# Optimization experiments

Hardware: AMD Instinct MI355X
Metric: run time of the kernel (lower is better)

The kernel has to match this reference:

```python
import jax, jax.numpy as jnp
import numpy as np

MODEL_DIM = 1024
NUM_HEADS = 16
HEAD_DIM = MODEL_DIM // NUM_HEADS


def setup_inputs() -> dict:
    key = jax.random.key(0)
    ks = jax.random.split(key, 9)
    s = 1.0 / np.sqrt(MODEL_DIM)
    d = {
        "query": jax.random.normal(ks[0], (2, 2048, MODEL_DIM), dtype=jnp.float32),
        "Wq": jax.random.normal(ks[1], (MODEL_DIM, MODEL_DIM), dtype=jnp.float32) * s,
        "bq": jnp.zeros((MODEL_DIM,), dtype=jnp.float32),
        "Wk": jax.random.normal(ks[2], (MODEL_DIM, MODEL_DIM), dtype=jnp.float32) * s,
        "bk": jnp.zeros((MODEL_DIM,), dtype=jnp.float32),
        "Wv": jax.random.normal(ks[3], (MODEL_DIM, MODEL_DIM), dtype=jnp.float32) * s,
        "bv": jnp.zeros((MODEL_DIM,), dtype=jnp.float32),
        "Wo": jax.random.normal(ks[4], (MODEL_DIM, MODEL_DIM), dtype=jnp.float32) * s,
        "bo": jnp.zeros((MODEL_DIM,), dtype=jnp.float32),
    }
    return d


def reference(query, Wq, bq, Wk, bk, Wv, bv, Wo, bo):
    B, S, D = query.shape
    H, hd = NUM_HEADS, HEAD_DIM
    # self-attention: key = value = query
    q = (query @ Wq.T + bq).reshape(B, S, H, hd).transpose(0, 2, 1, 3)  # [B,H,S,hd]
    k = (query @ Wk.T + bk).reshape(B, S, H, hd).transpose(0, 2, 1, 3)
    v = (query @ Wv.T + bv).reshape(B, S, H, hd).transpose(0, 2, 1, 3)
    scores = jnp.einsum("bhqd,bhkd->bhqk", q, k) / np.sqrt(hd)  # [B,H,S,S]
    attn = jax.nn.softmax(scores, axis=-1)
    ctx = jnp.einsum("bhqk,bhkd->bhqd", attn, v)  # [B,H,S,hd]
    ctx = ctx.transpose(0, 2, 1, 3).reshape(B, S, D)
    return ctx @ Wo.T + bo
```

## Files before the change

### kernel.cpp

```cpp
#include <hip/hip_runtime.h>

typedef __attribute__((ext_vector_type(8))) __bf16 bf16x8;
typedef __attribute__((ext_vector_type(8))) unsigned short ushort8;
typedef __attribute__((ext_vector_type(4))) unsigned short ushort4v;
typedef __attribute__((ext_vector_type(4))) float f32x4;
typedef __attribute__((ext_vector_type(2))) _Float16 f16x2;
typedef __attribute__((ext_vector_type(4))) _Float16 f16x4;
typedef __attribute__((ext_vector_type(8))) _Float16 f16x8;
typedef __attribute__((ext_vector_type(2))) __fp16 fp16v2;

__device__ __forceinline__ unsigned short f2bf(float f) {
    union { float f; unsigned int u; } c; c.f = f;
    unsigned int u = c.u;
    u += 0x7fffu + ((u >> 16) & 1u);
    return (unsigned short)(u >> 16);
}

__device__ __forceinline__ void async16(const void* g, void* l) {
    __builtin_amdgcn_global_load_lds(
        (const __attribute__((address_space(1))) unsigned int*)g,
        (__attribute__((address_space(3))) unsigned int*)l, 16, 0, 0);
}

__global__ __launch_bounds__(256) void cvt_all(
    const float* __restrict__ q,  const float* __restrict__ wq,
    const float* __restrict__ wk, const float* __restrict__ wv,
    const float* __restrict__ wo,
    unsigned short* __restrict__ q_bf, unsigned short* __restrict__ wqkv,
    unsigned short* __restrict__ wo_bf, float scale_k)
{
    const int NQ = 4096 * 1024, NW = 1024 * 1024;
    int i = (blockIdx.x * 256 + threadIdx.x) * 4;
    const float* src; unsigned short* dst; float sc = 1.0f; int off;
    if (i < NQ)               { src = q;  dst = q_bf;          off = i; }
    else if (i < NQ + NW)     { src = wq; dst = wqkv;          off = i - NQ; }
    else if (i < NQ + 2 * NW) { src = wk; dst = wqkv + NW;     off = i - NQ - NW; sc = scale_k; }
    else if (i < NQ + 3 * NW) { src = wv; dst = wqkv + 2 * NW; off = i - NQ - 2 * NW; }
    else                      { src = wo; dst = wo_bf;         off = i - NQ - 3 * NW; }
    float4 v = *(const float4*)(src + off);
    ushort4v o;
    o[0] = f2bf(v.x * sc); o[1] = f2bf(v.y * sc);
    o[2] = f2bf(v.z * sc); o[3] = f2bf(v.w * sc);
    *(ushort4v*)(dst + off) = o;
}

__global__ __launch_bounds__(256) void qkv_gemm(
    const unsigned short* __restrict__ A,
    const unsigned short* __restrict__ B,
    unsigned short* __restrict__ qkv,
    _Float16* __restrict__ vtg,
    const float* __restrict__ b0, const float* __restrict__ b1, const float* __restrict__ b2,
    float s1)
{
    __shared__ __align__(16) unsigned short As[128 * 64];
    __shared__ __align__(16) unsigned short Bs[128 * 64];

    const int tid  = threadIdx.x;
    const int lane = tid & 63, wave = tid >> 6;
    const int quad = lane >> 4, l15 = lane & 15;
    const int wm = wave >> 1, wn = wave & 1;
    const int by = blockIdx.y, bx = blockIdx.x;
    const int K = 1024;

    const int srow = lane >> 3;
    const int sp   = lane & 7;
    const int scl  = sp ^ srow;
    const int sw   = l15 & 7;

    f32x4 acc[4][4];
#pragma unroll
    for (int i = 0; i < 4; ++i)
#pragma unroll
        for (int j = 0; j < 4; ++j) acc[i][j] = (f32x4)(0.0f);

    for (int kt = 0; kt < 16; ++kt) {
        __syncthreads();
#pragma unroll
        for (int j = 0; j < 4; ++j) {
            int r0 = wave * 32 + j * 8;
            async16(A + (size_t)(by * 128 + r0 + srow) * K + kt * 64 + scl * 8, &As[r0 * 64]);
            async16(B + (size_t)(bx * 128 + r0 + srow) * K + kt * 64 + scl * 8, &Bs[r0 * 64]);
        }
        __syncthreads();

#pragma unroll
        for (int kh = 0; kh < 2; ++kh) {
            bf16x8 af[4], bfr[4];
#pragma unroll
            for (int mi = 0; mi < 4; ++mi)
                af[mi] = __builtin_bit_cast(bf16x8,
                    *(const ushort8*)&As[(wm * 64 + mi * 16 + l15) * 64 + ((kh * 4 + quad) ^ sw) * 8]);
#pragma unroll
            for (int ni = 0; ni < 4; ++ni)
                bfr[ni] = __builtin_bit_cast(bf16x8,
                    *(const ushort8*)&Bs[(wn * 64 + ni * 16 + l15) * 64 + ((kh * 4 + quad) ^ sw) * 8]);
#pragma unroll
            for (int mi = 0; mi < 4; ++mi)
#pragma unroll
                for (int ni = 0; ni < 4; ++ni)
                    acc[mi][ni] = __builtin_amdgcn_mfma_f32_16x16x32_bf16(af[mi], bfr[ni], acc[mi][ni], 0, 0, 0);
        }
    }

    if (bx < 16) {
#pragma unroll
        for (int ni = 0; ni < 4; ++ni) {
            int n = bx * 128 + wn * 64 + ni * 16 + l15;
            float bias = (n < 1024) ? b0[n] : b1[n - 1024] * s1;
#pragma unroll
            for (int mi = 0; mi < 4; ++mi) {
#pragma unroll
                for (int r = 0; r < 4; ++r) {
                    int m = by * 128 + wm * 64 + mi * 16 + quad * 4 + r;
                    qkv[(size_t)m * 2048 + n] = f2bf(acc[mi][ni][r] + bias);
                }
            }
        }
    } else {
        const int mb = by * 128 + wm * 64;
        const int b  = mb >> 11;
        const int st = (mb & 2047) >> 6;
#pragma unroll
        for (int ni = 0; ni < 4; ++ni) {
            int vf = (bx - 16) * 128 + wn * 64 + ni * 16 + l15;
            int h = vf >> 6, hd = vf & 63;
            float bias = b2[vf];
            _Float16* vrow = vtg + ((size_t)((b * 16 + h) * 64 + hd)) * 2048 + st * 64;
#pragma unroll
            for (int mi = 0; mi < 4; ++mi) {
                int p = ((mi >> 1) * 4 + quad) ^ (l15 & 7);
                f16x4 o;
#pragma unroll
                for (int r = 0; r < 4; ++r) o[r] = (_Float16)(acc[mi][ni][r] + bias);
                *(f16x4*)(vrow + p * 8 + (mi & 1) * 4) = o;
            }
        }
    }
}

__global__ __launch_bounds__(256) void out_gemm(
    const unsigned short* __restrict__ A,
    const unsigned short* __restrict__ B,
    float* __restrict__ Cout,
    const float* __restrict__ bo)
{
    __shared__ __align__(16) unsigned short As[128 * 64];
    __shared__ __align__(16) unsigned short Bs[64 * 64];

    const int tid  = threadIdx.x;
    const int lane = tid & 63, wave = tid >> 6;
    const int quad = lane >> 4, l15 = lane & 15;
    const int wm = wave >> 1, wn = wave & 1;
    const int by = blockIdx.y, bx = blockIdx.x;
    const int K = 1024;

    const int srow = lane >> 3;
    const int sp   = lane & 7;
    const int scl  = sp ^ srow;
    const int sw   = l15 & 7;

    f32x4 acc[4][2];
#pragma unroll
    for (int i = 0; i < 4; ++i)
#pragma unroll
        for (int j = 0; j < 2; ++j) acc[i][j] = (f32x4)(0.0f);

    for (int kt = 0; kt < 16; ++kt) {
        __syncthreads();
#pragma unroll
        for (int j = 0; j < 4; ++j) {
            int r0 = wave * 32 + j * 8;
            async16(A + (size_t)(by * 128 + r0 + srow) * K + kt * 64 + scl * 8, &As[r0 * 64]);
        }
#pragma unroll
        for (int j = 0; j < 2; ++j) {
            int r0 = wave * 16 + j * 8;
            async16(B + (size_t)(bx * 64 + r0 + srow) * K + kt * 64 + scl * 8, &Bs[r0 * 64]);
        }
        __syncthreads();

#pragma unroll
        for (int kh = 0; kh < 2; ++kh) {
            bf16x8 af[4], bfr[2];
#pragma unroll
            for (int mi = 0; mi < 4; ++mi)
                af[mi] = __builtin_bit_cast(bf16x8,
                    *(const ushort8*)&As[(wm * 64 + mi * 16 + l15) * 64 + ((kh * 4 + quad) ^ sw) * 8]);
#pragma unroll
            for (int ni = 0; ni < 2; ++ni)
                bfr[ni] = __builtin_bit_cast(bf16x8,
                    *(const ushort8*)&Bs[(wn * 32 + ni * 16 + l15) * 64 + ((kh * 4 + quad) ^ sw) * 8]);
#pragma unroll
            for (int mi = 0; mi < 4; ++mi)
#pragma unroll
                for (int ni = 0; ni < 2; ++ni)
                    acc[mi][ni] = __builtin_amdgcn_mfma_f32_16x16x32_bf16(af[mi], bfr[ni], acc[mi][ni], 0, 0, 0);
        }
    }

#pragma unroll
    for (int ni = 0; ni < 2; ++ni) {
        int n = bx * 64 + wn * 32 + ni * 16 + l15;
        float bias = bo[n];
#pragma unroll
        for (int mi = 0; mi < 4; ++mi) {
#pragma unroll
            for (int r = 0; r < 4; ++r) {
                int m = by * 128 + wm * 64 + mi * 16 + quad * 4 + r;
                Cout[(size_t)m * 1024 + n] = acc[mi][ni][r] + bias;
            }
        }
    }
}

__global__ __launch_bounds__(256, 2) void attn(const unsigned short* __restrict__ qkv,
                                               const _Float16* __restrict__ vtg,
                                               unsigned short* __restrict__ ctx)
{
    __shared__ __align__(16) char smem[65536];

    const int tid  = threadIdx.x;
    const int lane = tid & 63, wave = tid >> 6;
    const int quad = lane >> 4, l15 = lane & 15;
    const int bh = blockIdx.y;
    const int b = bh >> 4, h = bh & 15;
    const int q0 = blockIdx.x * 64;

    const int srow = lane >> 3;
    const int sp   = lane & 7;
    const int scl  = sp ^ srow;
    const int sw   = l15 & 7;

    unsigned short* KsW = (unsigned short*)(smem + wave * 16384);
    _Float16*       VtW = (_Float16*)(smem + wave * 16384 + 8192);

    bf16x8 qf[4][2];
#pragma unroll
    for (int s = 0; s < 4; ++s) {
        int qrow = b * 2048 + q0 + s * 16 + l15;
#pragma unroll
        for (int kh = 0; kh < 2; ++kh)
            qf[s][kh] = __builtin_bit_cast(bf16x8,
                *(const ushort8*)(qkv + (size_t)qrow * 2048 + h * 64 + kh * 32 + quad * 8));
    }

    f32x4 ot[4][4];
#pragma unroll
    for (int s = 0; s < 4; ++s)
#pragma unroll
        for (int ht = 0; ht < 4; ++ht) ot[s][ht] = (f32x4)(0.0f);
    float l_acc[4] = {0.0f, 0.0f, 0.0f, 0.0f};
    const fp16v2 ones = {(__fp16)1.0f, (__fp16)1.0f};

    for (int t = 0; t < 8; ++t) {
        int kt = wave * 8 + t;
#pragma unroll
        for (int j = 0; j < 8; ++j) {
            int row = j * 8 + srow;
            async16(qkv + (size_t)(b * 2048 + kt * 64 + row) * 2048 + 1024 + h * 64 + scl * 8,
                    &KsW[j * 8 * 64]);
            async16(vtg + (size_t)(bh * 64 + row) * 2048 + kt * 64 + sp * 8,
                    (unsigned short*)&VtW[j * 8 * 64]);
        }
        asm volatile("s_waitcnt vmcnt(0)" ::: "memory");
        __builtin_amdgcn_sched_barrier(0);

        f16x4 pv[4][4];
#pragma unroll
        for (int mt = 0; mt < 4; ++mt) {
            const unsigned short* kb = &KsW[(mt * 16 + l15) * 64];
            bf16x8 k0 = __builtin_bit_cast(bf16x8, *(const ushort8*)(kb + (quad ^ sw) * 8));
            bf16x8 k1 = __builtin_bit_cast(bf16x8, *(const ushort8*)(kb + ((quad ^ sw) ^ 4) * 8));
#pragma unroll
            for (int s = 0; s < 4; ++s) {
                f32x4 s4 = (f32x4)(0.0f);
                s4 = __builtin_amdgcn_mfma_f32_16x16x32_bf16(k0, qf[s][0], s4, 0, 0, 0);
                s4 = __builtin_amdgcn_mfma_f32_16x16x32_bf16(k1, qf[s][1], s4, 0, 0, 0);
                float p0 = __builtin_amdgcn_exp2f(s4[0]);
                float p1 = __builtin_amdgcn_exp2f(s4[1]);
                float p2 = __builtin_amdgcn_exp2f(s4[2]);
                float p3 = __builtin_amdgcn_exp2f(s4[3]);
                fp16v2 lo = __builtin_amdgcn_cvt_pkrtz(p0, p1);
                fp16v2 hi = __builtin_amdgcn_cvt_pkrtz(p2, p3);
                l_acc[s] = __builtin_amdgcn_fdot2(lo, ones, l_acc[s], false);
                l_acc[s] = __builtin_amdgcn_fdot2(hi, ones, l_acc[s], false);
                f16x2 lo2 = __builtin_bit_cast(f16x2, lo);
                f16x2 hi2 = __builtin_bit_cast(f16x2, hi);
                pv[s][mt] = __builtin_shufflevector(lo2, hi2, 0, 1, 2, 3);
            }
        }

#pragma unroll
        for (int ht = 0; ht < 4; ++ht) {
            const _Float16* vb = &VtW[(ht * 16 + l15) * 64];
#pragma unroll
            for (int g = 0; g < 2; ++g) {
                f16x8 v8 = *(const f16x8*)(vb + (((g * 4 + quad) ^ sw)) * 8);
                f16x4 vlo = __builtin_shufflevector(v8, v8, 0, 1, 2, 3);
                f16x4 vhi = __builtin_shufflevector(v8, v8, 4, 5, 6, 7);
#pragma unroll
                for (int s = 0; s < 4; ++s) {
                    ot[s][ht] = __builtin_amdgcn_mfma_f32_16x16x16f16(vlo, pv[s][2 * g],     ot[s][ht], 0, 0, 0);
                    ot[s][ht] = __builtin_amdgcn_mfma_f32_16x16x16f16(vhi, pv[s][2 * g + 1], ot[s][ht], 0, 0, 0);
                }
            }
        }
    }

    float lred[4];
#pragma unroll
    for (int s = 0; s < 4; ++s) {
        float l = l_acc[s];
        l += __shfl_xor(l, 16, 64);
        l += __shfl_xor(l, 32, 64);
        lred[s] = l;
    }

    __syncthreads();
    float* lsh = (float*)smem;
    if (quad == 0) {
#pragma unroll
        for (int s = 0; s < 4; ++s) lsh[wave * 64 + s * 16 + l15] = lred[s];
    }
    __syncthreads();
    int myrow = wave * 16 + l15;
    float lt = lsh[0 * 64 + myrow] + lsh[1 * 64 + myrow] + lsh[2 * 64 + myrow] + lsh[3 * 64 + myrow];
    float inv = 1.0f / lt;

    __syncthreads();
    float* red = (float*)smem;
#pragma unroll
    for (int s = 0; s < 4; ++s) {
#pragma unroll
        for (int ht = 0; ht < 4; ++ht) {
            int c = (ht * 4 + quad) ^ l15;
            *(f32x4*)(red + wave * 4096 + (s * 16 + l15) * 64 + c * 4) = ot[s][ht];
        }
    }
    __syncthreads();
    {
        int qrow = b * 2048 + q0 + myrow;
#pragma unroll
        for (int ht = 0; ht < 4; ++ht) {
            int c = (ht * 4 + quad) ^ l15;
            f32x4 ssum = *(const f32x4*)(red + 0 * 4096 + myrow * 64 + c * 4);
#pragma unroll
            for (int w2 = 1; w2 < 4; ++w2)
                ssum += *(const f32x4*)(red + w2 * 4096 + myrow * 64 + c * 4);
            ushort4v o4;
#pragma unroll
            for (int r = 0; r < 4; ++r) o4[r] = f2bf(ssum[r] * inv);
            *(ushort4v*)(ctx + (size_t)qrow * 1024 + h * 64 + ht * 16 + quad * 4) = o4;
        }
    }
}

extern "C" void kernel_launch(void* const* d_in, const int* in_sizes, int n_in,
                              void* d_out, int out_size, void* d_ws, size_t ws_size,
                              hipStream_t stream) {
    const float* query = (const float*)d_in[0];
    const float* Wq = (const float*)d_in[1];
    const float* bq = (const float*)d_in[2];
    const float* Wk = (const float*)d_in[3];
    const float* bk = (const float*)d_in[4];
    const float* Wv = (const float*)d_in[5];
    const float* bv = (const float*)d_in[6];
    const float* Wo = (const float*)d_in[7];
    const float* bo = (const float*)d_in[8];

    char* ws = (char*)d_ws;
    unsigned short* q_bf  = (unsigned short*)(ws);
    unsigned short* ctx   = (unsigned short*)(ws);
    unsigned short* wqkv  = (unsigned short*)(ws + 8388608);
    unsigned short* wo_bf = (unsigned short*)(ws + 14680064);
    unsigned short* qkv   = (unsigned short*)(ws + 16777216);
    _Float16*       vtg   = (_Float16*)(ws + 33554432);

    const float SCALE = 0.125f * 1.4426950408889634f;

    cvt_all<<<8192, 256, 0, stream>>>(query, Wq, Wk, Wv, Wo, q_bf, wqkv, wo_bf, SCALE);
    qkv_gemm<<<dim3(24, 32), 256, 0, stream>>>(q_bf, wqkv, qkv, vtg, bq, bk, bv, SCALE);
    attn<<<dim3(32, 32), 256, 0, stream>>>(qkv, vtg, ctx);
    out_gemm<<<dim3(16, 32), 256, 0, stream>>>(ctx, wo_bf, (float*)d_out, bo);
}
```

Measured before the change: 199.3 us.

## Double-buffer V tiles and load K directly to registers in attention loop

Reworks the attention inner loop to double-buffer V tiles in LDS, using the space K previously occupied. K fragments are now loaded straight from global memory into registers instead of through LDS. The next tile's loads are issued before the current tile is computed, with partial vmcnt waits, so memory latency overlaps MFMA/exp work. This costs more registers for two K sets and depends on the hand-counted vmcnt values (16) matching the number of outstanding loads exactly.

```diff
diff --git a/kernel.cpp b/kernel.cpp
--- a/kernel.cpp
+++ b/kernel.cpp
@@ -213,6 +213,19 @@
     }
 }
 
+struct KSet { bf16x8 f[4][2]; };
+
+__device__ __forceinline__ void loadK(const unsigned short* __restrict__ qkv,
+                                      int b, int h, int kt, int l15, int quad, KSet& ks) {
+#pragma unroll
+    for (int mt = 0; mt < 4; ++mt) {
+        const unsigned short* kr =
+            qkv + (size_t)(b * 2048 + kt * 64 + mt * 16 + l15) * 2048 + 1024 + h * 64;
+        ks.f[mt][0] = __builtin_bit_cast(bf16x8, *(const ushort8*)(kr + quad * 8));
+        ks.f[mt][1] = __builtin_bit_cast(bf16x8, *(const ushort8*)(kr + 32 + quad * 8));
+    }
+}
+
 __global__ __launch_bounds__(256, 2) void attn(const unsigned short* __restrict__ qkv,
                                                const _Float16* __restrict__ vtg,
                                                unsigned short* __restrict__ ctx)
@@ -228,11 +241,10 @@
 
     const int srow = lane >> 3;
     const int sp   = lane & 7;
-    const int scl  = sp ^ srow;
     const int sw   = l15 & 7;
 
-    unsigned short* KsW = (unsigned short*)(smem + wave * 16384);
-    _Float16*       VtW = (_Float16*)(smem + wave * 16384 + 8192);
+    _Float16* VtW[2] = { (_Float16*)(smem + wave * 16384),
+                         (_Float16*)(smem + wave * 16384 + 8192) };
 
     bf16x8 qf[4][2];
 #pragma unroll
@@ -252,30 +264,24 @@
     float l_acc[4] = {0.0f, 0.0f, 0.0f, 0.0f};
     const fp16v2 ones = {(__fp16)1.0f, (__fp16)1.0f};
 
-    for (int t = 0; t < 8; ++t) {
-        int kt = wave * 8 + t;
+    auto issueV = [&](int t, int vb) {
 #pragma unroll
         for (int j = 0; j < 8; ++j) {
             int row = j * 8 + srow;
-            async16(qkv + (size_t)(b * 2048 + kt * 64 + row) * 2048 + 1024 + h * 64 + scl * 8,
-                    &KsW[j * 8 * 64]);
-            async16(vtg + (size_t)(bh * 64 + row) * 2048 + kt * 64 + sp * 8,
-                    (unsigned short*)&VtW[j * 8 * 64]);
-        }
-        asm volatile("s_waitcnt vmcnt(0)" ::: "memory");
-        __builtin_amdgcn_sched_barrier(0);
-
+            async16(vtg + (size_t)(bh * 64 + row) * 2048 + (wave * 8 + t) * 64 + sp * 8,
+                    (unsigned short*)&VtW[vb][j * 8 * 64]);
+        }
+    };
+
+    auto computeTile = [&](const KSet& ks, const _Float16* Vt) {
         f16x4 pv[4][4];
 #pragma unroll
         for (int mt = 0; mt < 4; ++mt) {
-            const unsigned short* kb = &KsW[(mt * 16 + l15) * 64];
-            bf16x8 k0 = __builtin_bit_cast(bf16x8, *(const ushort8*)(kb + (quad ^ sw) * 8));
-            bf16x8 k1 = __builtin_bit_cast(bf16x8, *(const ushort8*)(kb + ((quad ^ sw) ^ 4) * 8));
 #pragma unroll
             for (int s = 0; s < 4; ++s) {
                 f32x4 s4 = (f32x4)(0.0f);
-                s4 = __builtin_amdgcn_mfma_f32_16x16x32_bf16(k0, qf[s][0], s4, 0, 0, 0);
-                s4 = __builtin_amdgcn_mfma_f32_16x16x32_bf16(k1, qf[s][1], s4, 0, 0, 0);
+                s4 = __builtin_amdgcn_mfma_f32_16x16x32_bf16(ks.f[mt][0], qf[s][0], s4, 0, 0, 0);
+                s4 = __builtin_amdgcn_mfma_f32_16x16x32_bf16(ks.f[mt][1], qf[s][1], s4, 0, 0, 0);
                 float p0 = __builtin_amdgcn_exp2f(s4[0]);
                 float p1 = __builtin_amdgcn_exp2f(s4[1]);
                 float p2 = __builtin_amdgcn_exp2f(s4[2]);
@@ -289,10 +295,9 @@
                 pv[s][mt] = __builtin_shufflevector(lo2, hi2, 0, 1, 2, 3);
             }
         }
-
 #pragma unroll
         for (int ht = 0; ht < 4; ++ht) {
-            const _Float16* vb = &VtW[(ht * 16 + l15) * 64];
+            const _Float16* vb = &Vt[(ht * 16 + l15) * 64];
 #pragma unroll
             for (int g = 0; g < 2; ++g) {
                 f16x8 v8 = *(const f16x8*)(vb + (((g * 4 + quad) ^ sw)) * 8);
@@ -305,6 +310,28 @@
                 }
             }
         }
+    };
+
+    KSet kA, kB;
+    issueV(0, 0);
+    loadK(qkv, b, h, wave * 8 + 0, l15, quad, kA);
+
+    for (int tt = 0; tt < 4; ++tt) {
+        issueV(2 * tt + 1, 1);
+        loadK(qkv, b, h, wave * 8 + 2 * tt + 1, l15, quad, kB);
+        asm volatile("s_waitcnt vmcnt(16)" ::: "memory");
+        __builtin_amdgcn_sched_barrier(0);
+        computeTile(kA, VtW[0]);
+
+        if (tt < 3) {
+            issueV(2 * tt + 2, 0);
+            loadK(qkv, b, h, wave * 8 + 2 * tt + 2, l15, quad, kA);
+            asm volatile("s_waitcnt vmcnt(16)" ::: "memory");
+        } else {
+            asm volatile("s_waitcnt vmcnt(0)" ::: "memory");
+        }
+        __builtin_amdgcn_sched_barrier(0);
+        computeTile(kB, VtW[1]);
     }
 
     float lred[4];
```

After: 218.5 us. 1.1x slower.
